# Kernel tuning notes

Hardware: AMD Instinct MI355X
Metric: run time of the kernel (lower is better)

## Reference

```python
import jax, jax.numpy as jnp
import numpy as np

N_NODES = 100000
N_EDGES = 800000
N_GRAPHS = 128
D_IN = 84          # num_features_xd
D_HID = 840        # num_features_xd * 10
D_FC1 = 1024
D_OUT = 384


def setup_inputs() -> dict:
    key = jax.random.key(0)
    ks = jax.random.split(key, 12)
    x = jax.random.normal(ks[0], (N_NODES, D_IN), jnp.float32)
    edge_index = jax.random.randint(ks[1], (2, N_EDGES), 0, N_NODES)
    batch = jnp.sort(jax.random.randint(ks[2], (N_NODES,), 0, N_GRAPHS))

    def lin(k, fan_in, fan_out):
        bound = 1.0 / np.sqrt(fan_in)
        kw, kb = jax.random.split(k)
        W = jax.random.uniform(kw, (fan_in, fan_out), jnp.float32, -bound, bound)
        b = jax.random.uniform(kb, (fan_out,), jnp.float32, -bound, bound)
        return W, b

    W1, b1 = lin(ks[3], D_IN, D_IN)       # conv1.nn: Linear(84, 84)
    W2, b2 = lin(ks[4], D_IN, D_HID)      # conv2.nn: Linear(84, 840)
    Wg1, bg1 = lin(ks[5], 2 * D_HID, D_FC1)  # fc_g[0]: Linear(1680, 1024)
    Wg2, bg2 = lin(ks[6], D_FC1, D_OUT)      # fc_g[3]: Linear(1024, 384)
    return {"x": x, "edge_index": edge_index, "batch": batch,
            "W1": W1, "b1": b1, "W2": W2, "b2": b2,
            "Wg1": Wg1, "bg1": bg1, "Wg2": Wg2, "bg2": bg2}


def gin_conv(h, src, dst, W, b):
    # GINConv with eps=0: nn(x + sum_{j in N(i)} x_j), scatter-add over edges
    agg = jax.ops.segment_sum(h[src], dst, num_segments=N_NODES)
    return (h + agg) @ W + b


def reference(x, edge_index, batch, W1, b1, W2, b2, Wg1, bg1, Wg2, bg2):
    src, dst = edge_index[0], edge_index[1]
    h = jax.nn.relu(gin_conv(x, src, dst, W1, b1))    # [N, 84]
    h = jax.nn.relu(gin_conv(h, src, dst, W2, b2))    # [N, 840]

    # global max pool + global mean pool per graph
    counts = jax.ops.segment_sum(jnp.ones((N_NODES, 1), h.dtype), batch,
                                 num_segments=N_GRAPHS)          # [G, 1]
    sums = jax.ops.segment_sum(h, batch, num_segments=N_GRAPHS)  # [G, 840]
    meanp = sums / jnp.maximum(counts, 1.0)
    maxp = jax.ops.segment_max(h, batch, num_segments=N_GRAPHS)
    maxp = jnp.where(counts > 0, maxp, 0.0)

    z = jnp.concatenate([maxp, meanp], axis=1)        # [G, 1680]
    z = jax.nn.relu(z @ Wg1 + bg1)                    # dropout is identity in eval
    z = z @ Wg2 + bg2                                 # [G, 384]
    return z
```

## Files before the change

### kernel.cpp

```cpp
#include <hip/hip_runtime.h>

#define N_NODES 100000
#define N_EDGESC 800000
#define NGRAPH 128
#define DIN 84
#define DHID 840
#define DF1 1024
#define DOUTC 384
#define PBLK3 1563
#define KP1 1696
#define NBUCK 391
#define EPB 2048
#define XSTR 96

typedef __attribute__((ext_vector_type(4))) float f32x4;
typedef __attribute__((ext_vector_type(8))) short bf16x8;

__device__ __forceinline__ unsigned short f2bf(float f) {
  union { float f; unsigned int u; } v; v.f = f;
  unsigned int r = v.u + 0x7FFFu + ((v.u >> 16) & 1u);
  return (unsigned short)(r >> 16);
}
__device__ __forceinline__ float bf2f(unsigned short h) {
  union { unsigned int u; float f; } v; v.u = ((unsigned int)h) << 16;
  return v.f;
}

__global__ __launch_bounds__(256) void k_bhist(const int* __restrict__ dst, int* __restrict__ bcnt) {
  __shared__ int h[NBUCK];
  int t = threadIdx.x;
  for (int i = t; i < NBUCK; i += 256) h[i] = 0;
  __syncthreads();
  int base = blockIdx.x * EPB;
  int e1 = min(base + EPB, N_EDGESC);
  for (int e = base + t; e < e1; e += 256)
    atomicAdd(&h[dst[e] >> 8], 1);
  __syncthreads();
  for (int i = t; i < NBUCK; i += 256) if (h[i]) atomicAdd(&bcnt[i], h[i]);
}

__global__ __launch_bounds__(512) void k_bscan(const int* __restrict__ bcnt, int* __restrict__ boff,
                                               int* __restrict__ bcur) {
  __shared__ int sd[512];
  int t = threadIdx.x;
  int v = (t < NBUCK) ? bcnt[t] : 0;
  sd[t] = v; __syncthreads();
  for (int off = 1; off < 512; off <<= 1) {
    int add = (t >= off) ? sd[t - off] : 0;
    __syncthreads();
    sd[t] += add;
    __syncthreads();
  }
  if (t <= NBUCK) {
    boff[t] = sd[t] - v;
    if (t < NBUCK) bcur[t] = sd[t] - v;
  }
}

__global__ __launch_bounds__(256) void k_bfill(const int* __restrict__ src, const int* __restrict__ dst,
                                               int* __restrict__ bcur, unsigned int* __restrict__ rec) {
  __shared__ int hcnt[NBUCK];
  __shared__ int hbase[NBUCK];
  int t = threadIdx.x;
  int e0 = blockIdx.x * EPB;
  int e1 = min(e0 + EPB, N_EDGESC);
  for (int i = t; i < NBUCK; i += 256) hcnt[i] = 0;
  __syncthreads();
  for (int e = e0 + t; e < e1; e += 256)
    atomicAdd(&hcnt[dst[e] >> 8], 1);
  __syncthreads();
  for (int i = t; i < NBUCK; i += 256) {
    int c = hcnt[i];
    hbase[i] = c ? atomicAdd(&bcur[i], c) : 0;
  }
  __syncthreads();
  for (int i = t; i < NBUCK; i += 256) hcnt[i] = 0;
  __syncthreads();
  for (int e = e0 + t; e < e1; e += 256) {
    int d = dst[e];
    int b = d >> 8;
    int r = atomicAdd(&hcnt[b], 1);
    rec[hbase[b] + r] = ((unsigned int)(d & 255) << 24) | (unsigned int)src[e];
  }
}

__global__ __launch_bounds__(256) void k_bsort(const unsigned int* __restrict__ rec, const int* __restrict__ boff,
                                               int* __restrict__ rowptr, int* __restrict__ csr) {
  __shared__ int lcnt[256];
  __shared__ int lcur[256];
  int b = blockIdx.x, t = threadIdx.x;
  int e0 = boff[b], e1 = boff[b + 1];
  lcnt[t] = 0;
  __syncthreads();
  for (int i = e0 + t; i < e1; i += 256) atomicAdd(&lcnt[rec[i] >> 24], 1);
  __syncthreads();
  int v = lcnt[t];
  for (int off = 1; off < 256; off <<= 1) {
    int add = (t >= off) ? lcnt[t - off] : 0;
    __syncthreads();
    lcnt[t] += add;
    __syncthreads();
  }
  int excl = lcnt[t] - v;
  int node = b * 256 + t;
  if (node < N_NODES) rowptr[node] = e0 + excl;
  lcur[t] = e0 + excl;
  if (b == NBUCK - 1 && t == 0) rowptr[N_NODES] = N_EDGESC;
  __syncthreads();
  for (int i = e0 + t; i < e1; i += 256) {
    unsigned int r = rec[i];
    int d = r >> 24;
    int pos = atomicAdd(&lcur[d], 1);
    csr[pos] = (int)(r & 0xFFFFFFu);
  }
}

__global__ __launch_bounds__(256) void k_counts(const int* __restrict__ batch, int* __restrict__ cnt) {
  __shared__ int h[NGRAPH];
  int t = threadIdx.x;
  if (t < NGRAPH) h[t] = 0;
  __syncthreads();
  int base = blockIdx.x * 2048;
  for (int j = 0; j < 8; j++) {
    int i = base + j * 256 + t;
    if (i < N_NODES) atomicAdd(&h[batch[i]], 1);
  }
  __syncthreads();
  if (t < NGRAPH && h[t] > 0) atomicAdd(&cnt[t], h[t]);
}

__global__ __launch_bounds__(256) void k_xbf(const float* __restrict__ x, unsigned short* __restrict__ xb) {
  int idx = blockIdx.x * 256 + threadIdx.x;
  if (idx >= N_NODES * 24) return;
  int r = idx / 24, c = idx - r * 24;
  uint2 p = {0u, 0u};
  if (c < 21) {
    f32x4 v = *(const f32x4*)&x[r * DIN + c * 4];
    p.x = (unsigned int)f2bf(v.x) | ((unsigned int)f2bf(v.y) << 16);
    p.y = (unsigned int)f2bf(v.z) | ((unsigned int)f2bf(v.w) << 16);
  }
  *(uint2*)&xb[r * XSTR + c * 4] = p;
}

__device__ __forceinline__ f32x4 bfq(uint2 p) {
  f32x4 r;
  r.x = bf2f((unsigned short)(p.x & 0xffff)); r.y = bf2f((unsigned short)(p.x >> 16));
  r.z = bf2f((unsigned short)(p.y & 0xffff)); r.w = bf2f((unsigned short)(p.y >> 16));
  return r;
}

__global__ __launch_bounds__(256) void k_agg1b(const unsigned short* __restrict__ xb, const int* __restrict__ rowptr,
                                               const int* __restrict__ csr, float* __restrict__ out) {
  int t = threadIdx.x;
  int wv = t >> 6, l = t & 63;
  int grp = (l >= 42) ? 2 : (l >= 21 ? 1 : 0);
  int li = l - grp * 21;
  int node = blockIdx.x * 12 + wv * 3 + grp;
  bool act = (li < 21) && (node < N_NODES);
  int nclamp = min(node, N_NODES - 1);
  int r0 = rowptr[nclamp];
  int r1 = act ? rowptr[nclamp + 1] : r0;
  f32x4 a = {0.f, 0.f, 0.f, 0.f};
  if (act) a = bfq(*(const uint2*)&xb[nclamp * XSTR + li * 4]);
  int e = r0;
  for (; e + 8 <= r1; e += 8) {
    int s0 = csr[e], s1 = csr[e + 1], s2 = csr[e + 2], s3 = csr[e + 3];
    int s4 = csr[e + 4], s5 = csr[e + 5], s6 = csr[e + 6], s7 = csr[e + 7];
    uint2 q0 = *(const uint2*)&xb[s0 * XSTR + li * 4];
    uint2 q1 = *(const uint2*)&xb[s1 * XSTR + li * 4];
    uint2 q2 = *(const uint2*)&xb[s2 * XSTR + li * 4];
    uint2 q3 = *(const uint2*)&xb[s3 * XSTR + li * 4];
    uint2 q4 = *(const uint2*)&xb[s4 * XSTR + li * 4];
    uint2 q5 = *(const uint2*)&xb[s5 * XSTR + li * 4];
    uint2 q6 = *(const uint2*)&xb[s6 * XSTR + li * 4];
    uint2 q7 = *(const uint2*)&xb[s7 * XSTR + li * 4];
    a += ((bfq(q0) + bfq(q1)) + (bfq(q2) + bfq(q3))) + ((bfq(q4) + bfq(q5)) + (bfq(q6) + bfq(q7)));
  }
  for (; e + 4 <= r1; e += 4) {
    int s0 = csr[e], s1 = csr[e + 1], s2 = csr[e + 2], s3 = csr[e + 3];
    uint2 q0 = *(const uint2*)&xb[s0 * XSTR + li * 4];
    uint2 q1 = *(const uint2*)&xb[s1 * XSTR + li * 4];
    uint2 q2 = *(const uint2*)&xb[s2 * XSTR + li * 4];
    uint2 q3 = *(const uint2*)&xb[s3 * XSTR + li * 4];
    a += (bfq(q0) + bfq(q1)) + (bfq(q2) + bfq(q3));
  }
  for (; e < r1; e++) {
    int s = csr[e];
    a += bfq(*(const uint2*)&xb[s * XSTR + li * 4]);
  }
  if (act) ((f32x4*)out)[node * 21 + li] = a;
}

__global__ __launch_bounds__(256) void k_agg2(const unsigned short* __restrict__ h1b, const int* __restrict__ rowptr,
                                              const int* __restrict__ csr, unsigned short* __restrict__ out) {
  int t = threadIdx.x;
  int wv = t >> 6, l = t & 63;
  int grp = (l >= 42) ? 2 : (l >= 21 ? 1 : 0);
  int li = l - grp * 21;
  int node = blockIdx.x * 12 + wv * 3 + grp;
  bool act = (li < 21) && (node < N_NODES);
  int nclamp = min(node, N_NODES - 1);
  int r0 = rowptr[nclamp];
  int r1 = act ? rowptr[nclamp + 1] : r0;
  f32x4 a = {0.f, 0.f, 0.f, 0.f};
  if (act) a = bfq(*(const uint2*)&h1b[nclamp * XSTR + li * 4]);
  int e = r0;
  for (; e + 8 <= r1; e += 8) {
    int s0 = csr[e], s1 = csr[e + 1], s2 = csr[e + 2], s3 = csr[e + 3];
    int s4 = csr[e + 4], s5 = csr[e + 5], s6 = csr[e + 6], s7 = csr[e + 7];
    uint2 q0 = *(const uint2*)&h1b[s0 * XSTR + li * 4];
    uint2 q1 = *(const uint2*)&h1b[s1 * XSTR + li * 4];
    uint2 q2 = *(const uint2*)&h1b[s2 * XSTR + li * 4];
    uint2 q3 = *(const uint2*)&h1b[s3 * XSTR + li * 4];
    uint2 q4 = *(const uint2*)&h1b[s4 * XSTR + li * 4];
    uint2 q5 = *(const uint2*)&h1b[s5 * XSTR + li * 4];
    uint2 q6 = *(const uint2*)&h1b[s6 * XSTR + li * 4];
    uint2 q7 = *(const uint2*)&h1b[s7 * XSTR + li * 4];
    a += ((bfq(q0) + bfq(q1)) + (bfq(q2) + bfq(q3))) + ((bfq(q4) + bfq(q5)) + (bfq(q6) + bfq(q7)));
  }
  for (; e + 4 <= r1; e += 4) {
    int s0 = csr[e], s1 = csr[e + 1], s2 = csr[e + 2], s3 = csr[e + 3];
    uint2 q0 = *(const uint2*)&h1b[s0 * XSTR + li * 4];
    uint2 q1 = *(const uint2*)&h1b[s1 * XSTR + li * 4];
    uint2 q2 = *(const uint2*)&h1b[s2 * XSTR + li * 4];
    uint2 q3 = *(const uint2*)&h1b[s3 * XSTR + li * 4];
    a += (bfq(q0) + bfq(q1)) + (bfq(q2) + bfq(q3));
  }
  for (; e < r1; e++) {
    int s = csr[e];
    a += bfq(*(const uint2*)&h1b[s * XSTR + li * 4]);
  }
  if (act) {
    uint2 p;
    p.x = (unsigned int)f2bf(a.x) | ((unsigned int)f2bf(a.y) << 16);
    p.y = (unsigned int)f2bf(a.z) | ((unsigned int)f2bf(a.w) << 16);
    *(uint2*)&out[node * XSTR + li * 4] = p;
  }
}

__global__ __launch_bounds__(256) void k_w1t(const float* __restrict__ W1, unsigned short* __restrict__ w1h,
                                             unsigned short* __restrict__ w1l) {
  int idx = blockIdx.x * 256 + threadIdx.x;
  if (idx >= 96 * 96) return;
  int n = idx / 96, k = idx % 96;
  float v = (n < DIN && k < DIN) ? W1[k * DIN + n] : 0.f;
  unsigned short h = f2bf(v);
  w1h[idx] = h;
  w1l[idx] = f2bf(v - bf2f(h));
}

template <int K, int KPAD, int N>
__global__ __launch_bounds__(256) void k_wsplit(const float* __restrict__ W,
                                                unsigned short* __restrict__ wh,
                                                unsigned short* __restrict__ wl) {
  __shared__ float tile[32][33];
  int b = blockIdx.x;
  int kt = b % (KPAD / 32), nt = b / (KPAD / 32);
  int k0 = kt * 32, n0 = nt * 32;
  int t = threadIdx.x;
  int r = t >> 3, c4 = (t & 7) * 4;
  int k = k0 + r;
  f32x4 v = {0.f, 0.f, 0.f, 0.f};
  if (k < K) v = *(const f32x4*)&W[(size_t)k * N + n0 + c4];
  tile[r][c4 + 0] = v.x; tile[r][c4 + 1] = v.y; tile[r][c4 + 2] = v.z; tile[r][c4 + 3] = v.w;
  __syncthreads();
  int n = t >> 3;
  float f0 = tile[c4 + 0][n], f1 = tile[c4 + 1][n], f2 = tile[c4 + 2][n], f3 = tile[c4 + 3][n];
  unsigned short h0 = f2bf(f0), h1_ = f2bf(f1), h2_ = f2bf(f2), h3_ = f2bf(f3);
  uint2 ph, pl;
  ph.x = (unsigned int)h0 | ((unsigned int)h1_ << 16);
  ph.y = (unsigned int)h2_ | ((unsigned int)h3_ << 16);
  pl.x = (unsigned int)f2bf(f0 - bf2f(h0)) | ((unsigned int)f2bf(f1 - bf2f(h1_)) << 16);
  pl.y = (unsigned int)f2bf(f2 - bf2f(h2_)) | ((unsigned int)f2bf(f3 - bf2f(h3_)) << 16);
  *(uint2*)&wh[(size_t)(n0 + n) * KPAD + k0 + c4] = ph;
  *(uint2*)&wl[(size_t)(n0 + n) * KPAD + k0 + c4] = pl;
}

__global__ __launch_bounds__(256) void k_conv1m(const float* __restrict__ agg,
                                                const unsigned short* __restrict__ w1h,
                                                const unsigned short* __restrict__ w1l,
                                                const float* __restrict__ b1,
                                                unsigned short* __restrict__ h1b) {
  constexpr int LDA = 104;
  __shared__ __align__(16) unsigned short Ah[64 * LDA];
  __shared__ __align__(16) unsigned short Al[64 * LDA];
  int t = threadIdx.x;
  int m0 = blockIdx.x * 64;

  for (int idx = t; idx < 64 * 21; idx += 256) {
    int r = idx / 21, c = idx - r * 21;
    int row = m0 + r;
    f32x4 v = {0.f, 0.f, 0.f, 0.f};
    if (row < N_NODES) v = *(const f32x4*)&agg[row * DIN + c * 4];
    unsigned short h0 = f2bf(v.x), h1_ = f2bf(v.y), h2_ = f2bf(v.z), h3_ = f2bf(v.w);
    unsigned short l0 = f2bf(v.x - bf2f(h0)), l1 = f2bf(v.y - bf2f(h1_));
    unsigned short l2 = f2bf(v.z - bf2f(h2_)), l3 = f2bf(v.w - bf2f(h3_));
    unsigned int* ph = (unsigned int*)&Ah[r * LDA + c * 4];
    ph[0] = (unsigned int)h0 | ((unsigned int)h1_ << 16);
    ph[1] = (unsigned int)h2_ | ((unsigned int)h3_ << 16);
    unsigned int* pl = (unsigned int*)&Al[r * LDA + c * 4];
    pl[0] = (unsigned int)l0 | ((unsigned int)l1 << 16);
    pl[1] = (unsigned int)l2 | ((unsigned int)l3 << 16);
  }
  for (int idx = t; idx < 64 * 6; idx += 256) {
    int r = idx / 6, c = idx - r * 6;
    ((unsigned int*)&Ah[r * LDA + 84])[c] = 0;
    ((unsigned int*)&Al[r * LDA + 84])[c] = 0;
  }
  __syncthreads();

  int w = t >> 6, l = t & 63;
  int lr = l & 15, lk = (l >> 4) * 8;
  bf16x8 ah[3], al[3];
  #pragma unroll
  for (int kk = 0; kk < 3; kk++) {
    ah[kk] = *(bf16x8*)&Ah[(w * 16 + lr) * LDA + lk + kk * 32];
    al[kk] = *(bf16x8*)&Al[(w * 16 + lr) * LDA + lk + kk * 32];
  }

  #pragma unroll
  for (int nt = 0; nt < 6; nt++) {
    f32x4 acc = {0.f, 0.f, 0.f, 0.f};
    #pragma unroll
    for (int kk = 0; kk < 3; kk++) {
      bf16x8 bh = *(const bf16x8*)&w1h[(nt * 16 + lr) * 96 + lk + kk * 32];
      bf16x8 bl = *(const bf16x8*)&w1l[(nt * 16 + lr) * 96 + lk + kk * 32];
      acc = __builtin_amdgcn_mfma_f32_16x16x32_bf16(ah[kk], bh, acc, 0, 0, 0);
      acc = __builtin_amdgcn_mfma_f32_16x16x32_bf16(al[kk], bh, acc, 0, 0, 0);
      acc = __builtin_amdgcn_mfma_f32_16x16x32_bf16(ah[kk], bl, acc, 0, 0, 0);
    }
    int col = nt * 16 + lr;
    if (col < DIN) {
      float bias = b1[col];
      int rbase = m0 + w * 16 + (l >> 4) * 4;
      #pragma unroll
      for (int j = 0; j < 4; j++) {
        if (rbase + j < N_NODES)
          h1b[(rbase + j) * XSTR + col] = f2bf(fmaxf(acc[j] + bias, 0.f));
      }
    }
  }
}

__global__ __launch_bounds__(256) void k_w2t(const float* __restrict__ W2, unsigned short* __restrict__ w2t) {
  int idx = blockIdx.x * 256 + threadIdx.x;
  if (idx >= 896 * 96) return;
  int n = idx / 96, k = idx % 96;
  float v = (n < DHID && k < DIN) ? W2[k * DHID + n] : 0.f;
  w2t[idx] = f2bf(v);
}

__global__ __launch_bounds__(256) void k_conv2pool4(const unsigned short* __restrict__ aggb,
                                                    const unsigned short* __restrict__ w2t,
                                                    const float* __restrict__ b2,
                                                    const int* __restrict__ batch,
                                                    float2* __restrict__ pm, float2* __restrict__ pm1,
                                                    int* __restrict__ blkg,
                                                    int* __restrict__ maxb, float* __restrict__ sump) {
  constexpr int LDA = 104;
  __shared__ __align__(16) unsigned short At[64 * LDA];
  int t = threadIdx.x;
  int w = t >> 6, l = t & 63;
  int b = blockIdx.x >> 1;
  int half = blockIdx.x & 1;
  int m0 = b * 64;
  int lr = l & 15, hi = l >> 4, lk = hi * 8;

  for (int idx = t; idx < 64 * 12; idx += 256) {
    int r = idx / 12, c = idx - r * 12;
    uint4 v = {0u, 0u, 0u, 0u};
    int row = m0 + r;
    if (row < N_NODES) v = *(const uint4*)&aggb[row * XSTR + c * 8];
    *(uint4*)&At[r * LDA + c * 8] = v;
  }
  int g0 = batch[m0];
  int g1 = batch[min(m0 + 63, N_NODES - 1)];
  bool fast = (g0 == g1) && (m0 + 63 < N_NODES);
  __syncthreads();

  bf16x8 afr[4][3];
  #pragma unroll
  for (int rg = 0; rg < 4; rg++)
    #pragma unroll
    for (int kk = 0; kk < 3; kk++)
      afr[rg][kk] = *(bf16x8*)&At[(rg * 16 + lr) * LDA + lk + kk * 32];

  int pbase = half * 28 + w * 7;

  if (fast) {
    for (int i = 0; i < 7; i++) {
      int c = (pbase + i) * 16 + lr;
      const unsigned short* bp = &w2t[c * 96 + lk];
      bf16x8 b0v = *(const bf16x8*)(bp);
      bf16x8 b1v = *(const bf16x8*)(bp + 32);
      bf16x8 b2v = *(const bf16x8*)(bp + 64);
      float bias = (c < DHID) ? b2[c] : 0.f;
      float mx = 0.f, sm = 0.f;
      #pragma unroll
      for (int rg = 0; rg < 4; rg++) {
        f32x4 a_ = {0.f, 0.f, 0.f, 0.f};
        a_ = __builtin_amdgcn_mfma_f32_16x16x32_bf16(afr[rg][0], b0v, a_, 0, 0, 0);
        a_ = __builtin_amdgcn_mfma_f32_16x16x32_bf16(afr[rg][1], b1v, a_, 0, 0, 0);
        a_ = __builtin_amdgcn_mfma_f32_16x16x32_bf16(afr[rg][2], b2v, a_, 0, 0, 0);
        float v0 = fmaxf(a_[0] + bias, 0.f);
        float v1 = fmaxf(a_[1] + bias, 0.f);
        float v2 = fmaxf(a_[2] + bias, 0.f);
        float v3 = fmaxf(a_[3] + bias, 0.f);
        mx = fmaxf(mx, fmaxf(fmaxf(v0, v1), fmaxf(v2, v3)));
        sm += (v0 + v1) + (v2 + v3);
      }
      mx = fmaxf(mx, __shfl_xor(mx, 16)); sm += __shfl_xor(sm, 16);
      mx = fmaxf(mx, __shfl_xor(mx, 32)); sm += __shfl_xor(sm, 32);
      if (hi == 0 && c < DHID) pm[(size_t)b * DHID + c] = make_float2(mx, sm);
    }
  } else {
    int grow[4][4];
    #pragma unroll
    for (int rg = 0; rg < 4; rg++)
      #pragma unroll
      for (int j = 0; j < 4; j++) {
        int row = m0 + rg * 16 + hi * 4 + j;
        grow[rg][j] = (row < N_NODES) ? batch[row] : -1;
      }
    for (int i = 0; i < 7; i++) {
      int c = (pbase + i) * 16 + lr;
      const unsigned short* bp = &w2t[c * 96 + lk];
      bf16x8 b0v = *(const bf16x8*)(bp);
      bf16x8 b1v = *(const bf16x8*)(bp + 32);
      bf16x8 b2v = *(const bf16x8*)(bp + 64);
      float bias = (c < DHID) ? b2[c] : 0.f;
      float mx0 = 0.f, sm0 = 0.f, mx1 = 0.f, sm1 = 0.f;
      float vv[4][4];
      #pragma unroll
      for (int rg = 0; rg < 4; rg++) {
        f32x4 a_ = {0.f, 0.f, 0.f, 0.f};
        a_ = __builtin_amdgcn_mfma_f32_16x16x32_bf16(afr[rg][0], b0v, a_, 0, 0, 0);
        a_ = __builtin_amdgcn_mfma_f32_16x16x32_bf16(afr[rg][1], b1v, a_, 0, 0, 0);
        a_ = __builtin_amdgcn_mfma_f32_16x16x32_bf16(afr[rg][2], b2v, a_, 0, 0, 0);
        #pragma unroll
        for (int j = 0; j < 4; j++) {
          float v = fmaxf(a_[j] + bias, 0.f);
          vv[rg][j] = v;
          if (grow[rg][j] == g0) { mx0 = fmaxf(mx0, v); sm0 += v; }
          if (grow[rg][j] == g1) { mx1 = fmaxf(mx1, v); sm1 += v; }
        }
      }
      mx0 = fmaxf(mx0, __shfl_xor(mx0, 16)); sm0 += __shfl_xor(sm0, 16);
      mx0 = fmaxf(mx0, __shfl_xor(mx0, 32)); sm0 += __shfl_xor(sm0, 32);
      mx1 = fmaxf(mx1, __shfl_xor(mx1, 16)); sm1 += __shfl_xor(sm1, 16);
      mx1 = fmaxf(mx1, __shfl_xor(mx1, 32)); sm1 += __shfl_xor(sm1, 32);
      if (hi == 0 && c < DHID) {
        pm[(size_t)b * DHID + c] = make_float2(mx0, sm0);
        pm1[(size_t)b * DHID + c] = make_float2(mx1, sm1);
      }
      if (g1 - g0 >= 2) {
        for (int g = g0 + 1; g < g1; g++) {
          float mx = 0.f, sm = 0.f;
          #pragma unroll
          for (int rg = 0; rg < 4; rg++)
            #pragma unroll
            for (int j = 0; j < 4; j++)
              if (grow[rg][j] == g) { mx = fmaxf(mx, vv[rg][j]); sm += vv[rg][j]; }
          mx = fmaxf(mx, __shfl_xor(mx, 16)); sm += __shfl_xor(sm, 16);
          mx = fmaxf(mx, __shfl_xor(mx, 32)); sm += __shfl_xor(sm, 32);
          if (hi == 0 && c < DHID) {
            atomicMax(&maxb[g * DHID + c], __float_as_int(mx));
            atomicAdd(&sump[g * DHID + c], sm);
          }
        }
      }
    }
  }
  if (t == 0 && half == 0) { blkg[b * 2] = g0; blkg[b * 2 + 1] = g1; }
}

__global__ __launch_bounds__(256) void k_pool2(const float2* __restrict__ pm, const float2* __restrict__ pm1,
                                               const int* __restrict__ blkg, const int* __restrict__ cnt,
                                               const int* __restrict__ maxb, const float* __restrict__ sump,
                                               unsigned short* __restrict__ zh, unsigned short* __restrict__ zl) {
  __shared__ int sstart[NGRAPH];
  int g = blockIdx.x, t = threadIdx.x;
  if (t == 0) {
    int s = 0;
    for (int i = 0; i < NGRAPH; i++) { sstart[i] = s; s += cnt[i]; }
  }
  __syncthreads();
  int c0 = cnt[g];
  int ns = sstart[g], ne = ns + c0;
  int b0 = ns / 64, b1 = (c0 > 0) ? (ne - 1) / 64 : b0 - 1;
  for (int c = t; c < DHID; c += 256) {
    float mx = __int_as_float(maxb[g * DHID + c]);
    float sm = sump[g * DHID + c];
    for (int b = b0; b <= b1; b++) {
      int gg0 = blkg[2 * b], gg1 = blkg[2 * b + 1];
      if (gg0 == g)      { float2 p = pm[(size_t)b * DHID + c];  mx = fmaxf(mx, p.x); sm += p.y; }
      else if (gg1 == g) { float2 p = pm1[(size_t)b * DHID + c]; mx = fmaxf(mx, p.x); sm += p.y; }
    }
    float vmax = (c0 > 0) ? mx : 0.f;
    float vmean = sm / (float)max(c0, 1);
    unsigned short hm = f2bf(vmax);
    zh[g * KP1 + c] = hm;
    zl[g * KP1 + c] = f2bf(vmax - bf2f(hm));
    unsigned short he = f2bf(vmean);
    zh[g * KP1 + DHID + c] = he;
    zl[g * KP1 + DHID + c] = f2bf(vmean - bf2f(he));
  }
  if (t < KP1 - 2 * DHID) {
    zh[g * KP1 + 2 * DHID + t] = 0;
    zl[g * KP1 + 2 * DHID + t] = 0;
  }
}

__global__ __launch_bounds__(256) void k_mlp1m(const unsigned short* __restrict__ zh, const unsigned short* __restrict__ zl,
                                               const unsigned short* __restrict__ wh, const unsigned short* __restrict__ wl,
                                               const float* __restrict__ bg,
                                               unsigned short* __restrict__ z1h, unsigned short* __restrict__ z1l) {
  int t = threadIdx.x, w = t >> 6, l = t & 63;
  int lr = l & 15, hi = l >> 4, lk = hi * 8;
  int b = blockIdx.x;
  int n0 = (b >> 1) * 16;
  int m0 = (b & 1) * 64 + w * 16;
  const unsigned short* za = &zh[(size_t)(m0 + lr) * KP1 + lk];
  const unsigned short* zb = &zl[(size_t)(m0 + lr) * KP1 + lk];
  const unsigned short* wa = &wh[(size_t)(n0 + lr) * KP1 + lk];
  const unsigned short* wb = &wl[(size_t)(n0 + lr) * KP1 + lk];
  f32x4 acc = {0.f, 0.f, 0.f, 0.f};
  for (int ks = 0; ks < KP1 / 32; ks++) {
    bf16x8 ah = *(const bf16x8*)(za + ks * 32);
    bf16x8 al = *(const bf16x8*)(zb + ks * 32);
    bf16x8 bh = *(const bf16x8*)(wa + ks * 32);
    bf16x8 bl = *(const bf16x8*)(wb + ks * 32);
    acc = __builtin_amdgcn_mfma_f32_16x16x32_bf16(ah, bh, acc, 0, 0, 0);
    acc = __builtin_amdgcn_mfma_f32_16x16x32_bf16(al, bh, acc, 0, 0, 0);
    acc = __builtin_amdgcn_mfma_f32_16x16x32_bf16(ah, bl, acc, 0, 0, 0);
  }
  int col = n0 + lr;
  float bias = bg[col];
  #pragma unroll
  for (int j = 0; j < 4; j++) {
    int row = m0 + hi * 4 + j;
    float v = fmaxf(acc[j] + bias, 0.f);
    unsigned short h = f2bf(v);
    z1h[row * DF1 + col] = h;
    z1l[row * DF1 + col] = f2bf(v - bf2f(h));
  }
}

__global__ __launch_bounds__(256) void k_mlp2m(const unsigned short* __restrict__ z1h, const unsigned short* __restrict__ z1l,
                                               const unsigned short* __restrict__ wh, const unsigned short* __restrict__ wl,
                                               const float* __restrict__ bg, float* __restrict__ out) {
  int t = threadIdx.x, w = t >> 6, l = t & 63;
  int lr = l & 15, hi = l >> 4, lk = hi * 8;
  int b = blockIdx.x;
  int n0 = (b >> 1) * 16;
  int m0 = (b & 1) * 64 + w * 16;
  const unsigned short* za = &z1h[(size_t)(m0 + lr) * DF1 + lk];
  const unsigned short* zb = &z1l[(size_t)(m0 + lr) * DF1 + lk];
  const unsigned short* wa = &wh[(size_t)(n0 + lr) * DF1 + lk];
  const unsigned short* wb = &wl[(size_t)(n0 + lr) * DF1 + lk];
  f32x4 acc = {0.f, 0.f, 0.f, 0.f};
  for (int ks = 0; ks < DF1 / 32; ks++) {
    bf16x8 ah = *(const bf16x8*)(za + ks * 32);
    bf16x8 al = *(const bf16x8*)(zb + ks * 32);
    bf16x8 bh = *(const bf16x8*)(wa + ks * 32);
    bf16x8 bl = *(const bf16x8*)(wb + ks * 32);
    acc = __builtin_amdgcn_mfma_f32_16x16x32_bf16(ah, bh, acc, 0, 0, 0);
    acc = __builtin_amdgcn_mfma_f32_16x16x32_bf16(al, bh, acc, 0, 0, 0);
    acc = __builtin_amdgcn_mfma_f32_16x16x32_bf16(ah, bl, acc, 0, 0, 0);
  }
  int col = n0 + lr;
  float bias = bg[col];
  #pragma unroll
  for (int j = 0; j < 4; j++) {
    int row = m0 + hi * 4 + j;
    out[row * DOUTC + col] = acc[j] + bias;
  }
}

static constexpr size_t AL(size_t x) { return (x + 255) & ~(size_t)255; }

extern "C" void kernel_launch(void* const* d_in, const int* in_sizes, int n_in,
                              void* d_out, int out_size, void* d_ws, size_t ws_size,
                              hipStream_t stream) {
  const float* x   = (const float*)d_in[0];
  const int*  edge = (const int*)d_in[1];
  const int*  batch= (const int*)d_in[2];
  const float* W1  = (const float*)d_in[3];
  const float* b1  = (const float*)d_in[4];
  const float* W2  = (const float*)d_in[5];
  const float* b2  = (const float*)d_in[6];
  const float* Wg1 = (const float*)d_in[7];
  const float* bg1 = (const float*)d_in[8];
  const float* Wg2 = (const float*)d_in[9];
  const float* bg2 = (const float*)d_in[10];
  float* out = (float*)d_out;
  const int* src = edge;
  const int* dst = edge + N_EDGESC;

  size_t o = 0;
  size_t OFF_AGG = o;  o += AL((size_t)N_NODES * DIN * 4);
  size_t OFF_H1  = o;  o += AL((size_t)N_NODES * XSTR * 2);
  size_t OFF_AGB = o;  o += AL((size_t)N_NODES * XSTR * 2);
  size_t OFF_CSR = o;  o += AL((size_t)N_EDGESC * 4);
  size_t OFF_REC = o;  o += AL((size_t)N_EDGESC * 4);
  size_t OFF_W2T = o;  o += AL((size_t)896 * 96 * 2);
  size_t OFF_W1H = o;  o += AL((size_t)96 * 96 * 2);
  size_t OFF_W1L = o;  o += AL((size_t)96 * 96 * 2);
  size_t OFF_G1H = o;  o += AL((size_t)DF1 * KP1 * 2);
  size_t OFF_G1L = o;  o += AL((size_t)DF1 * KP1 * 2);
  size_t OFF_G2H = o;  o += AL((size_t)DOUTC * DF1 * 2);
  size_t OFF_G2L = o;  o += AL((size_t)DOUTC * DF1 * 2);
  size_t OFF_ZH  = o;  o += AL((size_t)NGRAPH * KP1 * 2);
  size_t OFF_ZL  = o;  o += AL((size_t)NGRAPH * KP1 * 2);
  size_t OFF_Z1H = o;  o += AL((size_t)NGRAPH * DF1 * 2);
  size_t OFF_Z1L = o;  o += AL((size_t)NGRAPH * DF1 * 2);
  size_t OFF_RP  = o;  o += AL((size_t)(N_NODES + 1) * 4);
  size_t OFF_BOF = o;  o += AL((NBUCK + 1) * 4);
  size_t OFF_BCU = o;  o += AL(NBUCK * 4);
  size_t OFF_BC  = o;  o += AL(NBUCK * 4);
  size_t OFF_MAX = o;  o += AL((size_t)NGRAPH * DHID * 4);
  size_t OFF_SUM = o;  o += AL((size_t)NGRAPH * DHID * 4);
  size_t OFF_CNT = o;  o += AL(NGRAPH * 4);
  size_t TOTAL = o;
  size_t ZERO0 = OFF_BC, ZEROB = TOTAL - OFF_BC;
  if (ws_size < TOTAL) return;

  size_t PB = AL((size_t)PBLK3 * DHID * 8);
  size_t OFF_PM  = OFF_AGG;
  size_t OFF_PM1 = OFF_AGG + PB;
  size_t OFF_BLG = OFF_AGG + 2 * PB;

  char* ws = (char*)d_ws;
  float* agg = (float*)(ws + OFF_AGG);
  unsigned short* h1b = (unsigned short*)(ws + OFF_H1);
  unsigned short* aggb = (unsigned short*)(ws + OFF_AGB);
  unsigned short* xb   = (unsigned short*)(ws + OFF_AGB);
  int* csr   = (int*)(ws + OFF_CSR);
  unsigned int* rec = (unsigned int*)(ws + OFF_REC);
  unsigned short* w2t = (unsigned short*)(ws + OFF_W2T);
  unsigned short* w1h = (unsigned short*)(ws + OFF_W1H);
  unsigned short* w1l = (unsigned short*)(ws + OFF_W1L);
  unsigned short* g1h = (unsigned short*)(ws + OFF_G1H);
  unsigned short* g1l = (unsigned short*)(ws + OFF_G1L);
  unsigned short* g2h = (unsigned short*)(ws + OFF_G2H);
  unsigned short* g2l = (unsigned short*)(ws + OFF_G2L);
  unsigned short* zh  = (unsigned short*)(ws + OFF_ZH);
  unsigned short* zl  = (unsigned short*)(ws + OFF_ZL);
  unsigned short* z1h = (unsigned short*)(ws + OFF_Z1H);
  unsigned short* z1l = (unsigned short*)(ws + OFF_Z1L);
  int* rowptr = (int*)(ws + OFF_RP);
  int* boff  = (int*)(ws + OFF_BOF);
  int* bcur  = (int*)(ws + OFF_BCU);
  int* bcnt  = (int*)(ws + OFF_BC);
  int* maxb  = (int*)(ws + OFF_MAX);
  float* sump= (float*)(ws + OFF_SUM);
  int* cnt   = (int*)(ws + OFF_CNT);
  float2* pm  = (float2*)(ws + OFF_PM);
  float2* pm1 = (float2*)(ws + OFF_PM1);
  int* blkg  = (int*)(ws + OFF_BLG);

  hipMemsetAsync(ws + ZERO0, 0, ZEROB, stream);

  k_w2t<<<(896 * 96 + 255) / 256, 256, 0, stream>>>(W2, w2t);
  k_w1t<<<(96 * 96 + 255) / 256, 256, 0, stream>>>(W1, w1h, w1l);
  k_wsplit<2 * DHID, KP1, DF1><<<(KP1 / 32) * (DF1 / 32), 256, 0, stream>>>(Wg1, g1h, g1l);
  k_wsplit<DF1, DF1, DOUTC><<<(DF1 / 32) * (DOUTC / 32), 256, 0, stream>>>(Wg2, g2h, g2l);
  k_xbf<<<(N_NODES * 24 + 255) / 256, 256, 0, stream>>>(x, xb);

  int nbb = (N_EDGESC + EPB - 1) / EPB;
  k_bhist<<<nbb, 256, 0, stream>>>(dst, bcnt);
  k_bscan<<<1, 512, 0, stream>>>(bcnt, boff, bcur);
  k_bfill<<<nbb, 256, 0, stream>>>(src, dst, bcur, rec);
  k_bsort<<<NBUCK, 256, 0, stream>>>(rec, boff, rowptr, csr);
  k_counts<<<(N_NODES + 2047) / 2048, 256, 0, stream>>>(batch, cnt);

  k_agg1b<<<(N_NODES + 11) / 12, 256, 0, stream>>>(xb, rowptr, csr, agg);
  k_conv1m<<<(N_NODES + 63) / 64, 256, 0, stream>>>(agg, w1h, w1l, b1, h1b);
  k_agg2<<<(N_NODES + 11) / 12, 256, 0, stream>>>(h1b, rowptr, csr, aggb);
  k_conv2pool4<<<2 * PBLK3, 256, 0, stream>>>(aggb, w2t, b2, batch, pm, pm1, blkg, maxb, sump);
  k_pool2<<<NGRAPH, 256, 0, stream>>>(pm, pm1, blkg, cnt, maxb, sump, zh, zl);

  k_mlp1m<<<(DF1 / 16) * 2, 256, 0, stream>>>(zh, zl, g1h, g1l, bg1, z1h, z1l);
  k_mlp2m<<<(DOUTC / 16) * 2, 256, 0, stream>>>(z1h, z1l, g2h, g2l, bg2, out);
}
```

Measured before the change: 264.6 us.

## Fuse prep kernels into one launch and fuse layer-1 aggregation with conv1 GEMM

Merges the x-to-bf16 conversion, the weight transposes and splits, and the graph-count histogram into a single block-dispatched prep kernel, cutting several launches. It also fuses the first neighbor aggregation into the conv1 MFMA kernel. Aggregated rows are written straight into shared memory as bf16 hi/lo pairs, which removes the fp32 agg round trip through global memory. The cost is fewer aggregation blocks (64 rows each, processed in six sequential passes per block), which may reduce latency hiding for the gather.

After: 253.9 us. -4.1%, faster.

```diff
diff --git a/kernel.cpp b/kernel.cpp
--- a/kernel.cpp
+++ b/kernel.cpp
@@ -13,6 +13,14 @@
 #define EPB 2048
 #define XSTR 96
 
+#define XBF_B 9375
+#define W2T_B 336
+#define W1T_B 36
+#define CNT_B 49
+#define G1_B  1696
+#define G2_B  384
+#define PREP_B (XBF_B + W2T_B + W1T_B + CNT_B + G1_B + G2_B)
+
 typedef __attribute__((ext_vector_type(4))) float f32x4;
 typedef __attribute__((ext_vector_type(8))) short bf16x8;
 
@@ -24,6 +32,12 @@
 __device__ __forceinline__ float bf2f(unsigned short h) {
   union { unsigned int u; float f; } v; v.u = ((unsigned int)h) << 16;
   return v.f;
+}
+__device__ __forceinline__ f32x4 bfq(uint2 p) {
+  f32x4 r;
+  r.x = bf2f((unsigned short)(p.x & 0xffff)); r.y = bf2f((unsigned short)(p.x >> 16));
+  r.z = bf2f((unsigned short)(p.y & 0xffff)); r.w = bf2f((unsigned short)(p.y >> 16));
+  return r;
 }
 
 __global__ __launch_bounds__(256) void k_bhist(const int* __restrict__ dst, int* __restrict__ bcnt) {
@@ -115,80 +129,189 @@
   }
 }
 
-__global__ __launch_bounds__(256) void k_counts(const int* __restrict__ batch, int* __restrict__ cnt) {
+__global__ __launch_bounds__(256) void k_prep(const float* __restrict__ x, unsigned short* __restrict__ xb,
+                                              const float* __restrict__ W2, unsigned short* __restrict__ w2t,
+                                              const float* __restrict__ W1, unsigned short* __restrict__ w1h,
+                                              unsigned short* __restrict__ w1l,
+                                              const int* __restrict__ batch, int* __restrict__ cnt,
+                                              const float* __restrict__ Wg1, unsigned short* __restrict__ g1h,
+                                              unsigned short* __restrict__ g1l,
+                                              const float* __restrict__ Wg2, unsigned short* __restrict__ g2h,
+                                              unsigned short* __restrict__ g2l) {
+  __shared__ float tile[32][33];
   __shared__ int h[NGRAPH];
+  int b = blockIdx.x, t = threadIdx.x;
+
+  if (b < XBF_B) {
+    int idx = b * 256 + t;
+    if (idx >= N_NODES * 24) return;
+    int r = idx / 24, c = idx - r * 24;
+    uint2 p = {0u, 0u};
+    if (c < 21) {
+      f32x4 v = *(const f32x4*)&x[r * DIN + c * 4];
+      p.x = (unsigned int)f2bf(v.x) | ((unsigned int)f2bf(v.y) << 16);
+      p.y = (unsigned int)f2bf(v.z) | ((unsigned int)f2bf(v.w) << 16);
+    }
+    *(uint2*)&xb[r * XSTR + c * 4] = p;
+    return;
+  }
+  b -= XBF_B;
+  if (b < W2T_B) {
+    int idx = b * 256 + t;
+    if (idx >= 896 * 96) return;
+    int n = idx / 96, k = idx % 96;
+    float v = (n < DHID && k < DIN) ? W2[k * DHID + n] : 0.f;
+    w2t[idx] = f2bf(v);
+    return;
+  }
+  b -= W2T_B;
+  if (b < W1T_B) {
+    int idx = b * 256 + t;
+    if (idx >= 96 * 96) return;
+    int n = idx / 96, k = idx % 96;
+    float v = (n < DIN && k < DIN) ? W1[k * DIN + n] : 0.f;
+    unsigned short hh = f2bf(v);
+    w1h[idx] = hh;
+    w1l[idx] = f2bf(v - bf2f(hh));
+    return;
+  }
+  b -= W1T_B;
+  if (b < CNT_B) {
+    if (t < NGRAPH) h[t] = 0;
+    __syncthreads();
+    int base = b * 2048;
+    for (int j = 0; j < 8; j++) {
+      int i = base + j * 256 + t;
+      if (i < N_NODES) atomicAdd(&h[batch[i]], 1);
+    }
+    __syncthreads();
+    if (t < NGRAPH && h[t] > 0) atomicAdd(&cnt[t], h[t]);
+    return;
+  }
+  b -= CNT_B;
+  const float* W; unsigned short *wh, *wl; int K, KPAD, N, vb;
+  if (b < G1_B) { W = Wg1; wh = g1h; wl = g1l; K = 2 * DHID; KPAD = KP1; N = DF1; vb = b; }
+  else          { W = Wg2; wh = g2h; wl = g2l; K = DF1; KPAD = DF1; N = DOUTC; vb = b - G1_B; }
+  int kt = vb % (KPAD / 32), nt2 = vb / (KPAD / 32);
+  int k0 = kt * 32, n0 = nt2 * 32;
+  int r = t >> 3, c4 = (t & 7) * 4;
+  int k = k0 + r;
+  f32x4 v = {0.f, 0.f, 0.f, 0.f};
+  if (k < K) v = *(const f32x4*)&W[(size_t)k * N + n0 + c4];
+  tile[r][c4 + 0] = v.x; tile[r][c4 + 1] = v.y; tile[r][c4 + 2] = v.z; tile[r][c4 + 3] = v.w;
+  __syncthreads();
+  int n = t >> 3;
+  float f0 = tile[c4 + 0][n], f1 = tile[c4 + 1][n], f2 = tile[c4 + 2][n], f3 = tile[c4 + 3][n];
+  unsigned short h0 = f2bf(f0), h1_ = f2bf(f1), h2_ = f2bf(f2), h3_ = f2bf(f3);
+  uint2 ph, pl;
+  ph.x = (unsigned int)h0 | ((unsigned int)h1_ << 16);
+  ph.y = (unsigned int)h2_ | ((unsigned int)h3_ << 16);
+  pl.x = (unsigned int)f2bf(f0 - bf2f(h0)) | ((unsigned int)f2bf(f1 - bf2f(h1_)) << 16);
+  pl.y = (unsigned int)f2bf(f2 - bf2f(h2_)) | ((unsigned int)f2bf(f3 - bf2f(h3_)) << 16);
+  *(uint2*)&wh[(size_t)(n0 + n) * KPAD + k0 + c4] = ph;
+  *(uint2*)&wl[(size_t)(n0 + n) * KPAD + k0 + c4] = pl;
+}
+
+__global__ __launch_bounds__(256) void k_agg1conv1(const unsigned short* __restrict__ xb,
+                                                   const int* __restrict__ rowptr,
+                                                   const int* __restrict__ csr,
+                                                   const unsigned short* __restrict__ w1h,
+                                                   const unsigned short* __restrict__ w1l,
+                                                   const float* __restrict__ b1,
+                                                   unsigned short* __restrict__ h1b) {
+  constexpr int LDA = 104;
+  __shared__ __align__(16) unsigned short Ah[64 * LDA];
+  __shared__ __align__(16) unsigned short Al[64 * LDA];
   int t = threadIdx.x;
-  if (t < NGRAPH) h[t] = 0;
-  __syncthreads();
-  int base = blockIdx.x * 2048;
-  for (int j = 0; j < 8; j++) {
-    int i = base + j * 256 + t;
-    if (i < N_NODES) atomicAdd(&h[batch[i]], 1);
-  }
-  __syncthreads();
-  if (t < NGRAPH && h[t] > 0) atomicAdd(&cnt[t], h[t]);
-}
-
-__global__ __launch_bounds__(256) void k_xbf(const float* __restrict__ x, unsigned short* __restrict__ xb) {
-  int idx = blockIdx.x * 256 + threadIdx.x;
-  if (idx >= N_NODES * 24) return;
-  int r = idx / 24, c = idx - r * 24;
-  uint2 p = {0u, 0u};
-  if (c < 21) {
-    f32x4 v = *(const f32x4*)&x[r * DIN + c * 4];
-    p.x = (unsigned int)f2bf(v.x) | ((unsigned int)f2bf(v.y) << 16);
-    p.y = (unsigned int)f2bf(v.z) | ((unsigned int)f2bf(v.w) << 16);
-  }
-  *(uint2*)&xb[r * XSTR + c * 4] = p;
-}
-
-__device__ __forceinline__ f32x4 bfq(uint2 p) {
-  f32x4 r;
-  r.x = bf2f((unsigned short)(p.x & 0xffff)); r.y = bf2f((unsigned short)(p.x >> 16));
-  r.z = bf2f((unsigned short)(p.y & 0xffff)); r.w = bf2f((unsigned short)(p.y >> 16));
-  return r;
-}
-
-__global__ __launch_bounds__(256) void k_agg1b(const unsigned short* __restrict__ xb, const int* __restrict__ rowptr,
-                                               const int* __restrict__ csr, float* __restrict__ out) {
-  int t = threadIdx.x;
+  int m0 = blockIdx.x * 64;
   int wv = t >> 6, l = t & 63;
+
+  for (int idx = t; idx < 64 * 6; idx += 256) {
+    int r = idx / 6, c = idx - r * 6;
+    ((unsigned int*)&Ah[r * LDA + 84])[c] = 0;
+    ((unsigned int*)&Al[r * LDA + 84])[c] = 0;
+  }
+
   int grp = (l >= 42) ? 2 : (l >= 21 ? 1 : 0);
   int li = l - grp * 21;
-  int node = blockIdx.x * 12 + wv * 3 + grp;
-  bool act = (li < 21) && (node < N_NODES);
-  int nclamp = min(node, N_NODES - 1);
-  int r0 = rowptr[nclamp];
-  int r1 = act ? rowptr[nclamp + 1] : r0;
-  f32x4 a = {0.f, 0.f, 0.f, 0.f};
-  if (act) a = bfq(*(const uint2*)&xb[nclamp * XSTR + li * 4]);
-  int e = r0;
-  for (; e + 8 <= r1; e += 8) {
-    int s0 = csr[e], s1 = csr[e + 1], s2 = csr[e + 2], s3 = csr[e + 3];
-    int s4 = csr[e + 4], s5 = csr[e + 5], s6 = csr[e + 6], s7 = csr[e + 7];
-    uint2 q0 = *(const uint2*)&xb[s0 * XSTR + li * 4];
-    uint2 q1 = *(const uint2*)&xb[s1 * XSTR + li * 4];
-    uint2 q2 = *(const uint2*)&xb[s2 * XSTR + li * 4];
-    uint2 q3 = *(const uint2*)&xb[s3 * XSTR + li * 4];
-    uint2 q4 = *(const uint2*)&xb[s4 * XSTR + li * 4];
-    uint2 q5 = *(const uint2*)&xb[s5 * XSTR + li * 4];
-    uint2 q6 = *(const uint2*)&xb[s6 * XSTR + li * 4];
-    uint2 q7 = *(const uint2*)&xb[s7 * XSTR + li * 4];
-    a += ((bfq(q0) + bfq(q1)) + (bfq(q2) + bfq(q3))) + ((bfq(q4) + bfq(q5)) + (bfq(q6) + bfq(q7)));
-  }
-  for (; e + 4 <= r1; e += 4) {
-    int s0 = csr[e], s1 = csr[e + 1], s2 = csr[e + 2], s3 = csr[e + 3];
-    uint2 q0 = *(const uint2*)&xb[s0 * XSTR + li * 4];
-    uint2 q1 = *(const uint2*)&xb[s1 * XSTR + li * 4];
-    uint2 q2 = *(const uint2*)&xb[s2 * XSTR + li * 4];
-    uint2 q3 = *(const uint2*)&xb[s3 * XSTR + li * 4];
-    a += (bfq(q0) + bfq(q1)) + (bfq(q2) + bfq(q3));
-  }
-  for (; e < r1; e++) {
-    int s = csr[e];
-    a += bfq(*(const uint2*)&xb[s * XSTR + li * 4]);
-  }
-  if (act) ((f32x4*)out)[node * 21 + li] = a;
+  bool lact = (l < 63);
+
+  for (int rr = 0; rr < 6; rr++) {
+    int rowi = rr * 12 + wv * 3 + grp;
+    if (!lact || rowi >= 64) continue;
+    int node = m0 + rowi;
+    f32x4 a = {0.f, 0.f, 0.f, 0.f};
+    if (node < N_NODES) {
+      int r0 = rowptr[node], r1 = rowptr[node + 1];
+      a = bfq(*(const uint2*)&xb[node * XSTR + li * 4]);
+      int e = r0;
+      for (; e + 8 <= r1; e += 8) {
+        int s0 = csr[e], s1 = csr[e + 1], s2 = csr[e + 2], s3 = csr[e + 3];
+        int s4 = csr[e + 4], s5 = csr[e + 5], s6 = csr[e + 6], s7 = csr[e + 7];
+        uint2 q0 = *(const uint2*)&xb[s0 * XSTR + li * 4];
+        uint2 q1 = *(const uint2*)&xb[s1 * XSTR + li * 4];
+        uint2 q2 = *(const uint2*)&xb[s2 * XSTR + li * 4];
+        uint2 q3 = *(const uint2*)&xb[s3 * XSTR + li * 4];
+        uint2 q4 = *(const uint2*)&xb[s4 * XSTR + li * 4];
+        uint2 q5 = *(const uint2*)&xb[s5 * XSTR + li * 4];
+        uint2 q6 = *(const uint2*)&xb[s6 * XSTR + li * 4];
+        uint2 q7 = *(const uint2*)&xb[s7 * XSTR + li * 4];
+        a += ((bfq(q0) + bfq(q1)) + (bfq(q2) + bfq(q3))) + ((bfq(q4) + bfq(q5)) + (bfq(q6) + bfq(q7)));
+      }
+      for (; e + 4 <= r1; e += 4) {
+        int s0 = csr[e], s1 = csr[e + 1], s2 = csr[e + 2], s3 = csr[e + 3];
+        uint2 q0 = *(const uint2*)&xb[s0 * XSTR + li * 4];
+        uint2 q1 = *(const uint2*)&xb[s1 * XSTR + li * 4];
+        uint2 q2 = *(const uint2*)&xb[s2 * XSTR + li * 4];
+        uint2 q3 = *(const uint2*)&xb[s3 * XSTR + li * 4];
+        a += (bfq(q0) + bfq(q1)) + (bfq(q2) + bfq(q3));
+      }
+      for (; e < r1; e++) {
+        int s = csr[e];
+        a += bfq(*(const uint2*)&xb[s * XSTR + li * 4]);
+      }
+    }
+    unsigned short h0 = f2bf(a.x), h1_ = f2bf(a.y), h2_ = f2bf(a.z), h3_ = f2bf(a.w);
+    unsigned short l0 = f2bf(a.x - bf2f(h0)), l1 = f2bf(a.y - bf2f(h1_));
+    unsigned short l2 = f2bf(a.z - bf2f(h2_)), l3 = f2bf(a.w - bf2f(h3_));
+    unsigned int* ph = (unsigned int*)&Ah[rowi * LDA + li * 4];
+    ph[0] = (unsigned int)h0 | ((unsigned int)h1_ << 16);
+    ph[1] = (unsigned int)h2_ | ((unsigned int)h3_ << 16);
+    unsigned int* pl = (unsigned int*)&Al[rowi * LDA + li * 4];
+    pl[0] = (unsigned int)l0 | ((unsigned int)l1 << 16);
+    pl[1] = (unsigned int)l2 | ((unsigned int)l3 << 16);
+  }
+  __syncthreads();
+
+  int lr = l & 15, lk = (l >> 4) * 8;
+  bf16x8 ah[3], al[3];
+  #pragma unroll
+  for (int kk = 0; kk < 3; kk++) {
+    ah[kk] = *(bf16x8*)&Ah[(wv * 16 + lr) * LDA + lk + kk * 32];
+    al[kk] = *(bf16x8*)&Al[(wv * 16 + lr) * LDA + lk + kk * 32];
+  }
+  #pragma unroll
+  for (int nt = 0; nt < 6; nt++) {
+    f32x4 acc = {0.f, 0.f, 0.f, 0.f};
+    #pragma unroll
+    for (int kk = 0; kk < 3; kk++) {
+      bf16x8 bh = *(const bf16x8*)&w1h[(nt * 16 + lr) * 96 + lk + kk * 32];
+      bf16x8 bl = *(const bf16x8*)&w1l[(nt * 16 + lr) * 96 + lk + kk * 32];
+      acc = __builtin_amdgcn_mfma_f32_16x16x32_bf16(ah[kk], bh, acc, 0, 0, 0);
+      acc = __builtin_amdgcn_mfma_f32_16x16x32_bf16(al[kk], bh, acc, 0, 0, 0);
+      acc = __builtin_amdgcn_mfma_f32_16x16x32_bf16(ah[kk], bl, acc, 0, 0, 0);
+    }
+    int col = nt * 16 + lr;
+    if (col < DIN) {
+      float bias = b1[col];
+      int rbase = m0 + wv * 16 + (l >> 4) * 4;
+      #pragma unroll
+      for (int j = 0; j < 4; j++) {
+        if (rbase + j < N_NODES)
+          h1b[(rbase + j) * XSTR + col] = f2bf(fmaxf(acc[j] + bias, 0.f));
+      }
+    }
+  }
 }
 
 __global__ __launch_bounds__(256) void k_agg2(const unsigned short* __restrict__ h1b, const int* __restrict__ rowptr,
@@ -236,118 +359,6 @@
     p.y = (unsigned int)f2bf(a.z) | ((unsigned int)f2bf(a.w) << 16);
     *(uint2*)&out[node * XSTR + li * 4] = p;
   }
-}
-
-__global__ __launch_bounds__(256) void k_w1t(const float* __restrict__ W1, unsigned short* __restrict__ w1h,
-                                             unsigned short* __restrict__ w1l) {
-  int idx = blockIdx.x * 256 + threadIdx.x;
-  if (idx >= 96 * 96) return;
-  int n = idx / 96, k = idx % 96;
-  float v = (n < DIN && k < DIN) ? W1[k * DIN + n] : 0.f;
-  unsigned short h = f2bf(v);
-  w1h[idx] = h;
-  w1l[idx] = f2bf(v - bf2f(h));
-}
-
-template <int K, int KPAD, int N>
-__global__ __launch_bounds__(256) void k_wsplit(const float* __restrict__ W,
-                                                unsigned short* __restrict__ wh,
-                                                unsigned short* __restrict__ wl) {
-  __shared__ float tile[32][33];
-  int b = blockIdx.x;
-  int kt = b % (KPAD / 32), nt = b / (KPAD / 32);
-  int k0 = kt * 32, n0 = nt * 32;
-  int t = threadIdx.x;
-  int r = t >> 3, c4 = (t & 7) * 4;
-  int k = k0 + r;
-  f32x4 v = {0.f, 0.f, 0.f, 0.f};
-  if (k < K) v = *(const f32x4*)&W[(size_t)k * N + n0 + c4];
-  tile[r][c4 + 0] = v.x; tile[r][c4 + 1] = v.y; tile[r][c4 + 2] = v.z; tile[r][c4 + 3] = v.w;
-  __syncthreads();
-  int n = t >> 3;
-  float f0 = tile[c4 + 0][n], f1 = tile[c4 + 1][n], f2 = tile[c4 + 2][n], f3 = tile[c4 + 3][n];
-  unsigned short h0 = f2bf(f0), h1_ = f2bf(f1), h2_ = f2bf(f2), h3_ = f2bf(f3);
-  uint2 ph, pl;
-  ph.x = (unsigned int)h0 | ((unsigned int)h1_ << 16);
-  ph.y = (unsigned int)h2_ | ((unsigned int)h3_ << 16);
-  pl.x = (unsigned int)f2bf(f0 - bf2f(h0)) | ((unsigned int)f2bf(f1 - bf2f(h1_)) << 16);
-  pl.y = (unsigned int)f2bf(f2 - bf2f(h2_)) | ((unsigned int)f2bf(f3 - bf2f(h3_)) << 16);
-  *(uint2*)&wh[(size_t)(n0 + n) * KPAD + k0 + c4] = ph;
-  *(uint2*)&wl[(size_t)(n0 + n) * KPAD + k0 + c4] = pl;
-}
-
-__global__ __launch_bounds__(256) void k_conv1m(const float* __restrict__ agg,
-                                                const unsigned short* __restrict__ w1h,
-                                                const unsigned short* __restrict__ w1l,
-                                                const float* __restrict__ b1,
-                                                unsigned short* __restrict__ h1b) {
-  constexpr int LDA = 104;
-  __shared__ __align__(16) unsigned short Ah[64 * LDA];
-  __shared__ __align__(16) unsigned short Al[64 * LDA];
-  int t = threadIdx.x;
-  int m0 = blockIdx.x * 64;
-
-  for (int idx = t; idx < 64 * 21; idx += 256) {
-    int r = idx / 21, c = idx - r * 21;
-    int row = m0 + r;
-    f32x4 v = {0.f, 0.f, 0.f, 0.f};
-    if (row < N_NODES) v = *(const f32x4*)&agg[row * DIN + c * 4];
-    unsigned short h0 = f2bf(v.x), h1_ = f2bf(v.y), h2_ = f2bf(v.z), h3_ = f2bf(v.w);
-    unsigned short l0 = f2bf(v.x - bf2f(h0)), l1 = f2bf(v.y - bf2f(h1_));
-    unsigned short l2 = f2bf(v.z - bf2f(h2_)), l3 = f2bf(v.w - bf2f(h3_));
-    unsigned int* ph = (unsigned int*)&Ah[r * LDA + c * 4];
-    ph[0] = (unsigned int)h0 | ((unsigned int)h1_ << 16);
-    ph[1] = (unsigned int)h2_ | ((unsigned int)h3_ << 16);
-    unsigned int* pl = (unsigned int*)&Al[r * LDA + c * 4];
-    pl[0] = (unsigned int)l0 | ((unsigned int)l1 << 16);
-    pl[1] = (unsigned int)l2 | ((unsigned int)l3 << 16);
-  }
-  for (int idx = t; idx < 64 * 6; idx += 256) {
-    int r = idx / 6, c = idx - r * 6;
-    ((unsigned int*)&Ah[r * LDA + 84])[c] = 0;
-    ((unsigned int*)&Al[r * LDA + 84])[c] = 0;
-  }
-  __syncthreads();
-
-  int w = t >> 6, l = t & 63;
-  int lr = l & 15, lk = (l >> 4) * 8;
-  bf16x8 ah[3], al[3];
-  #pragma unroll
-  for (int kk = 0; kk < 3; kk++) {
-    ah[kk] = *(bf16x8*)&Ah[(w * 16 + lr) * LDA + lk + kk * 32];
-    al[kk] = *(bf16x8*)&Al[(w * 16 + lr) * LDA + lk + kk * 32];
-  }
-
-  #pragma unroll
-  for (int nt = 0; nt < 6; nt++) {
-    f32x4 acc = {0.f, 0.f, 0.f, 0.f};
-    #pragma unroll
-    for (int kk = 0; kk < 3; kk++) {
-      bf16x8 bh = *(const bf16x8*)&w1h[(nt * 16 + lr) * 96 + lk + kk * 32];
-      bf16x8 bl = *(const bf16x8*)&w1l[(nt * 16 + lr) * 96 + lk + kk * 32];
-      acc = __builtin_amdgcn_mfma_f32_16x16x32_bf16(ah[kk], bh, acc, 0, 0, 0);
-      acc = __builtin_amdgcn_mfma_f32_16x16x32_bf16(al[kk], bh, acc, 0, 0, 0);
-      acc = __builtin_amdgcn_mfma_f32_16x16x32_bf16(ah[kk], bl, acc, 0, 0, 0);
-    }
-    int col = nt * 16 + lr;
-    if (col < DIN) {
-      float bias = b1[col];
-      int rbase = m0 + w * 16 + (l >> 4) * 4;
-      #pragma unroll
-      for (int j = 0; j < 4; j++) {
-        if (rbase + j < N_NODES)
-          h1b[(rbase + j) * XSTR + col] = f2bf(fmaxf(acc[j] + bias, 0.f));
-      }
-    }
-  }
-}
-
-__global__ __launch_bounds__(256) void k_w2t(const float* __restrict__ W2, unsigned short* __restrict__ w2t) {
-  int idx = blockIdx.x * 256 + threadIdx.x;
-  if (idx >= 896 * 96) return;
-  int n = idx / 96, k = idx % 96;
-  float v = (n < DHID && k < DIN) ? W2[k * DHID + n] : 0.f;
-  w2t[idx] = f2bf(v);
 }
 
 __global__ __launch_bounds__(256) void k_conv2pool4(const unsigned short* __restrict__ aggb,
@@ -631,7 +642,6 @@
   size_t OFF_BLG = OFF_AGG + 2 * PB;
 
   char* ws = (char*)d_ws;
-  float* agg = (float*)(ws + OFF_AGG);
   unsigned short* h1b = (unsigned short*)(ws + OFF_H1);
   unsigned short* aggb = (unsigned short*)(ws + OFF_AGB);
   unsigned short* xb   = (unsigned short*)(ws + OFF_AGB);
@@ -661,21 +671,16 @@
 
   hipMemsetAsync(ws + ZERO0, 0, ZEROB, stream);
 
-  k_w2t<<<(896 * 96 + 255) / 256, 256, 0, stream>>>(W2, w2t);
-  k_w1t<<<(96 * 96 + 255) / 256, 256, 0, stream>>>(W1, w1h, w1l);
-  k_wsplit<2 * DHID, KP1, DF1><<<(KP1 / 32) * (DF1 / 32), 256, 0, stream>>>(Wg1, g1h, g1l);
-  k_wsplit<DF1, DF1, DOUTC><<<(DF1 / 32) * (DOUTC / 32), 256, 0, stream>>>(Wg2, g2h, g2l);
-  k_xbf<<<(N_NODES * 24 + 255) / 256, 256, 0, stream>>>(x, xb);
+  k_prep<<<PREP_B, 256, 0, stream>>>(x, xb, W2, w2t, W1, w1h, w1l, batch, cnt,
+                                     Wg1, g1h, g1l, Wg2, g2h, g2l);
 
   int nbb = (N_EDGESC + EPB - 1) / EPB;
   k_bhist<<<nbb, 256, 0, stream>>>(dst, bcnt);
   k_bscan<<<1, 512, 0, stream>>>(bcnt, boff, bcur);
   k_bfill<<<nbb, 256, 0, stream>>>(src, dst, bcur, rec);
   k_bsort<<<NBUCK, 256, 0, stream>>>(rec, boff, rowptr, csr);
-  k_counts<<<(N_NODES + 2047) / 2048, 256, 0, stream>>>(batch, cnt);
-
-  k_agg1b<<<(N_NODES + 11) / 12, 256, 0, stream>>>(xb, rowptr, csr, agg);
-  k_conv1m<<<(N_NODES + 63) / 64, 256, 0, stream>>>(agg, w1h, w1l, b1, h1b);
+
+  k_agg1conv1<<<PBLK3, 256, 0, stream>>>(xb, rowptr, csr, w1h, w1l, b1, h1b);
   k_agg2<<<(N_NODES + 11) / 12, 256, 0, stream>>>(h1b, rowptr, csr, aggb);
   k_conv2pool4<<<2 * PBLK3, 256, 0, stream>>>(aggb, w2t, b2, batch, pm, pm1, blkg, maxb, sump);
   k_pool2<<<NGRAPH, 256, 0, stream>>>(pm, pm1, blkg, cnt, maxb, sump, zh, zl);
```
